# Kernel optimization log

Hardware: AMD Instinct MI355X
Metric: run time of the kernel (lower is better)

The kernel has to match this reference:

```python
import jax, jax.numpy as jnp
import numpy as np

H, DH = 16, 64            # num heads, head dim
D = H * DH                # hidden size 1024
ALPHA, BW, A, R = 1.0, 1.0, 0.5, 1.0
D_INT = DH                # num_heads > 1 -> d_intrinsic = head_dim
EPS = 1e-12
CLIP = 1.0 - 1e-6         # keep acos (and its grad) finite


def setup_inputs() -> dict:
    key = jax.random.key(0)
    ks = jax.random.split(key, 5)
    w = lambda k: jax.random.normal(k, (D, D), jnp.float32) * 0.02
    return {
        "x": jax.random.normal(ks[0], (4, 1024, D), jnp.float32),
        "wq": w(ks[1]), "bq": jnp.zeros((D,), jnp.float32),
        "wk": w(ks[2]), "bk": jnp.zeros((D,), jnp.float32),
        "wv": w(ks[3]), "bv": jnp.zeros((D,), jnp.float32),
        "wo": w(ks[4]), "bo": jnp.zeros((D,), jnp.float32),
    }


def reference(x, wq, bq, wk, bk, wv, bv, wo, bo):
    B, S, _ = x.shape

    def heads(t):  # [B,S,D] -> [B,H,S,DH]
        return t.reshape(B, S, H, DH).transpose(0, 2, 1, 3)

    def l2norm(t):
        return t / jnp.maximum(jnp.linalg.norm(t, axis=-1, keepdims=True), EPS)

    q = l2norm(heads(x @ wq + bq))
    k = l2norm(heads(x @ wk + bk))
    v = heads(x @ wv + bv)

    # spherical geodesic distance
    dot = jnp.clip(jnp.einsum('bhqd,bhkd->bhqk', q, k), -CLIP, CLIP)
    g_dist = jnp.arccos(dot) * R

    # power-law kernel (alpha < 2 branch)
    attn_score = (1.0 + g_dist / jnp.sqrt(BW)) ** (-(D_INT + ALPHA))

    # bistochastic (Sinkhorn-like) normalization, a > 0 branch
    n_r = attn_score.sum(-1)   # [B,H,S] row sums
    n_c = attn_score.sum(-2)   # [B,H,S] col sums
    k_tilde = (n_r ** (-A))[..., :, None] * attn_score * (n_c ** (-A))[..., None, :]
    probs = k_tilde / jnp.maximum(k_tilde.sum(-1, keepdims=True), EPS)  # L1 row normalize

    out = jnp.einsum('bhqk,bhkd->bhqd', probs, v)
    out = out.transpose(0, 2, 1, 3).reshape(B, S, D)
    return out @ wo + bo
```

## Files before the change

### kernel.cpp

```cpp
#include <hip/hip_runtime.h>
#include <hip/hip_bf16.h>
#include <cstdint>
#include <cstddef>

#define BATCH  4
#define SEQ    1024
#define NHEAD  16
#define DHEAD  64
#define DMODEL 1024
#define NROWS  4096
#define BH     64
#define CLIPV  0.999999f
#define PEXP   65.0f

#define QOFF   133.5f
#define QK_    490.8988764f
#define QINV   0.0020370716f
#define QC     65535.5f

typedef _Float16 h16;
typedef _Float16 half8 __attribute__((ext_vector_type(8)));
typedef _Float16 half4 __attribute__((ext_vector_type(4)));
typedef __fp16   fp16x2 __attribute__((ext_vector_type(2)));
typedef float    f32x4 __attribute__((ext_vector_type(4)));
typedef unsigned uint2v __attribute__((ext_vector_type(2)));

typedef const __attribute__((address_space(1))) void gas_void;
typedef __attribute__((address_space(3))) void las_void;
#define GLOAD_LDS16(g, l) \
    __builtin_amdgcn_global_load_lds((gas_void*)(g), (las_void*)(l), 16, 0, 0)

__device__ __forceinline__ float spfns_lg(float d) {
    d = __builtin_amdgcn_fmed3f(d, -CLIPV, CLIPV);
    float a = fabsf(d);
    float s = __builtin_amdgcn_sqrtf(1.0f - a);
    float p = -0.0187293f;
    p = fmaf(p, a,  0.0742610f);
    p = fmaf(p, a, -0.2121144f);
    p = fmaf(p, a,  1.5707288f);
    float r = s * p;
    float g = (d >= 0.0f) ? r : (3.14159265358979f - r);
    return __builtin_amdgcn_logf(1.0f + g);
}

__device__ __forceinline__ unsigned pk_h2(float lo, float hi) {
    fp16x2 v = __builtin_amdgcn_cvt_pkrtz(lo, hi);
    return __builtin_bit_cast(unsigned, v);
}

__device__ __forceinline__ half8 h8_zero() {
    half8 z;
    #pragma unroll
    for (int e = 0; e < 8; ++e) z[e] = (h16)0.f;
    return z;
}

__global__ __launch_bounds__(256) void cvt_x(const float* __restrict__ x,
                                             h16* __restrict__ xh)
{
    size_t i = ((size_t)blockIdx.x * 256 + threadIdx.x) * 8;
    float4 a = *reinterpret_cast<const float4*>(&x[i]);
    float4 b = *reinterpret_cast<const float4*>(&x[i + 4]);
    half8 o;
    o[0]=(h16)a.x; o[1]=(h16)a.y; o[2]=(h16)a.z; o[3]=(h16)a.w;
    o[4]=(h16)b.x; o[5]=(h16)b.y; o[6]=(h16)b.z; o[7]=(h16)b.w;
    *reinterpret_cast<half8*>(&xh[i]) = o;
}

__global__ __launch_bounds__(256) void wtrans(const float* __restrict__ wq,
                                              const float* __restrict__ wk,
                                              const float* __restrict__ wv,
                                              const float* __restrict__ wo,
                                              h16* __restrict__ wt3,
                                              h16* __restrict__ wot)
{
    __shared__ float T[64][65];
    const int k0 = blockIdx.x * 64, d0 = blockIdx.y * 64, z = blockIdx.z;
    const float* src = (z==0)?wq:(z==1)?wk:(z==2)?wv:wo;
    h16* dst = (z==3) ? wot : (wt3 + (size_t)z * 1024 * 1024);
    const int t = threadIdx.x;

    #pragma unroll
    for (int p = 0; p < 4; ++p) {
        int k = (t >> 4) + p * 16;
        int c = (t & 15) * 4;
        float4 v = *reinterpret_cast<const float4*>(&src[(size_t)(k0 + k) * 1024 + d0 + c]);
        T[c + 0][k] = v.x; T[c + 1][k] = v.y; T[c + 2][k] = v.z; T[c + 3][k] = v.w;
    }
    __syncthreads();
    #pragma unroll
    for (int p = 0; p < 2; ++p) {
        int dl = (t >> 3) + p * 32;
        int c  = (t & 7) * 8;
        half8 o;
        #pragma unroll
        for (int e = 0; e < 8; ++e) o[e] = (h16)T[dl][c + e];
        *reinterpret_cast<half8*>(&dst[(size_t)(d0 + dl) * 1024 + k0 + c]) = o;
    }
}

__global__ __launch_bounds__(256) void gemm_f16(const h16* __restrict__ A,
                                                const h16* __restrict__ Bt,
                                                const float* __restrict__ b0,
                                                const float* __restrict__ b1,
                                                const float* __restrict__ b2,
                                                h16* __restrict__ oq,
                                                h16* __restrict__ ok,
                                                h16* __restrict__ ovt,
                                                float* __restrict__ of32,
                                                int mode)
{
    __shared__ __align__(16) h16 As[128][64];
    __shared__ __align__(16) h16 Bs[128][64];
    const int n0 = blockIdx.x * 128, d0 = blockIdx.y * 128;
    const int t = threadIdx.x, l = t & 63, w = t >> 6;
    const int wr = (w >> 1) * 64, wc = (w & 1) * 64;
    const int lr = l >> 3, lc8 = (l & 7) * 8;

    f32x4 acc[4][4];
    #pragma unroll
    for (int i = 0; i < 4; ++i)
        #pragma unroll
        for (int j = 0; j < 4; ++j) acc[i][j] = (f32x4){0.f,0.f,0.f,0.f};

    for (int k0 = 0; k0 < 1024; k0 += 64) {
        __syncthreads();
        #pragma unroll
        for (int q = 0; q < 4; ++q) {
            int r = w * 32 + q * 8;
            GLOAD_LDS16(&A[(size_t)(n0 + r + lr) * 1024 + k0 + lc8], &As[r][0]);
            GLOAD_LDS16(&Bt[(size_t)(d0 + r + lr) * 1024 + k0 + lc8], &Bs[r][0]);
        }
        __syncthreads();
        #pragma unroll
        for (int kk = 0; kk < 2; ++kk) {
            half8 a[4], b[4];
            #pragma unroll
            for (int fi = 0; fi < 4; ++fi)
                a[fi] = *reinterpret_cast<const half8*>(&As[wr + fi*16 + (l & 15)][((l >> 4) * 8) + kk * 32]);
            #pragma unroll
            for (int fj = 0; fj < 4; ++fj)
                b[fj] = *reinterpret_cast<const half8*>(&Bs[wc + fj*16 + (l & 15)][((l >> 4) * 8) + kk * 32]);
            #pragma unroll
            for (int fi = 0; fi < 4; ++fi)
                #pragma unroll
                for (int fj = 0; fj < 4; ++fj)
                    acc[fi][fj] = __builtin_amdgcn_mfma_f32_16x16x32_f16(a[fi], b[fj], acc[fi][fj], 0, 0, 0);
        }
    }

    if (mode == 0) {
        const int dbase = d0 + wc;
        const int mat = dbase >> 10, d1b = dbase & 1023, h = d1b >> 6;
        const float* bp = (mat == 0) ? b0 : (mat == 1) ? b1 : b2;
        #pragma unroll
        for (int fi = 0; fi < 4; ++fi) {
            float vals[4][4];
            #pragma unroll
            for (int fj = 0; fj < 4; ++fj) {
                float bias = bp[d1b + fj * 16 + (l & 15)];
                #pragma unroll
                for (int rr = 0; rr < 4; ++rr) vals[fj][rr] = acc[fi][fj][rr] + bias;
            }
            if (mat < 2) {
                float ss[4];
                #pragma unroll
                for (int rr = 0; rr < 4; ++rr)
                    ss[rr] = vals[0][rr]*vals[0][rr] + vals[1][rr]*vals[1][rr]
                           + vals[2][rr]*vals[2][rr] + vals[3][rr]*vals[3][rr];
                #pragma unroll
                for (int off = 1; off < 16; off <<= 1) {
                    #pragma unroll
                    for (int rr = 0; rr < 4; ++rr) ss[rr] += __shfl_xor(ss[rr], off);
                }
                #pragma unroll
                for (int rr = 0; rr < 4; ++rr) {
                    float sc = __builtin_amdgcn_rcpf(
                        fmaxf(__builtin_amdgcn_sqrtf(ss[rr]), 1e-12f));
                    #pragma unroll
                    for (int fj = 0; fj < 4; ++fj) vals[fj][rr] *= sc;
                }
            }
            const int s0n = n0 + wr + fi * 16 + ((l >> 4) << 2);
            #pragma unroll
            for (int fj = 0; fj < 4; ++fj) {
                int dh = fj * 16 + (l & 15);
                if (mat == 2) {
                    int b = s0n >> 10, s0 = s0n & 1023;
                    half4 o;
                    #pragma unroll
                    for (int rr = 0; rr < 4; ++rr) o[rr] = (h16)vals[fj][rr];
                    *reinterpret_cast<half4*>(&ovt[(((size_t)(b * NHEAD + h)) * DHEAD + dh) * SEQ + s0]) = o;
                } else {
                    h16* dst = (mat == 0) ? oq : ok;
                    #pragma unroll
                    for (int rr = 0; rr < 4; ++rr) {
                        int n = s0n + rr, b = n >> 10, s = n & 1023;
                        dst[(((size_t)(b * NHEAD + h)) * SEQ + s) * DHEAD + dh] = (h16)vals[fj][rr];
                    }
                }
            }
        }
    } else {
        #pragma unroll
        for (int fi = 0; fi < 4; ++fi) {
            #pragma unroll
            for (int fj = 0; fj < 4; ++fj) {
                int d = d0 + wc + fj * 16 + (l & 15);
                int s0n = n0 + wr + fi * 16 + ((l >> 4) << 2);
                float bias = b0[d];
                #pragma unroll
                for (int rr = 0; rr < 4; ++rr) {
                    int n = s0n + rr;
                    of32[(size_t)n * DMODEL + d] = acc[fi][fj][rr] + bias;
                }
            }
        }
    }
}

template<int CACHED>
__global__ __launch_bounds__(256) void passA(const h16* __restrict__ qh,
                                             const h16* __restrict__ kh,
                                             float* __restrict__ nc,
                                             unsigned* __restrict__ rm_u,
                                             int* __restrict__ gacc,
                                             unsigned short* __restrict__ Sw)
{
    __shared__ __align__(16) h16 Ks[32][72];
    __shared__ float red[4][32];
    const int t = threadIdx.x, l = t & 63, w = t >> 6;
    const int id  = blockIdx.y * 32 + blockIdx.x;
    const int nid = (id & 7) * 256 + (id >> 3);
    const int jt = nid & 31, bh = nid >> 5;
    const int j0 = jt * 32;

    {
        int r = t >> 3, c = (t & 7) * 8;
        *reinterpret_cast<half8*>(&Ks[r][c]) =
            *reinterpret_cast<const half8*>(&kh[(((size_t)bh * SEQ) + j0 + r) * DHEAD + c]);
    }
    __syncthreads();

    half8 kfr[2][2];
    #pragma unroll
    for (int f = 0; f < 2; ++f)
        #pragma unroll
        for (int kk = 0; kk < 2; ++kk)
            kfr[f][kk] = *reinterpret_cast<const half8*>(&Ks[f*16 + (l & 15)][((l >> 4) * 8) + kk * 32]);

    float ncacc[8];
    #pragma unroll
    for (int x = 0; x < 8; ++x) ncacc[x] = 0.f;

    unsigned short* sp[2] = {nullptr, nullptr};
    if (CACHED) {
        size_t base = ((((size_t)(bh*16 + (jt >> 1))*16)*16 + w*4 + (jt & 1)*2) << 8)
                      + (size_t)l*4;
        sp[0] = Sw + base;
        sp[1] = sp[0] + 256;
    }

    const h16* qb = qh + ((size_t)bh * SEQ + w*16 + (l & 15)) * DHEAD + ((l >> 4) * 8);
    half8 nq0 = *reinterpret_cast<const half8*>(qb);
    half8 nq1 = *reinterpret_cast<const half8*>(qb + 32);

    #pragma unroll 2
    for (int it = 0; it < 16; ++it) {
        half8 aq0 = nq0, aq1 = nq1;
        if (it < 15) {
            const h16* qn = qb + (size_t)(it + 1) * 64 * DHEAD;
            nq0 = *reinterpret_cast<const half8*>(qn);
            nq1 = *reinterpret_cast<const half8*>(qn + 32);
        }

        float mloc = 1e30f;
        #pragma unroll
        for (int f = 0; f < 2; ++f) {
            f32x4 cfr = (f32x4){0.f,0.f,0.f,0.f};
            cfr = __builtin_amdgcn_mfma_f32_16x16x32_f16(kfr[f][0], aq0, cfr, 0, 0, 0);
            cfr = __builtin_amdgcn_mfma_f32_16x16x32_f16(kfr[f][1], aq1, cfr, 0, 0, 0);
            unsigned uq[4];
            #pragma unroll
            for (int rr = 0; rr < 4; ++rr) {
                float lg = spfns_lg(cfr[rr]);
                float tt = lg * (-PEXP);
                ncacc[f*4 + rr] += __builtin_amdgcn_exp2f(tt);
                mloc = fminf(mloc, lg);
                if (CACHED) uq[rr] = (unsigned)fmaf(tt, QK_, QC);
            }
            if (CACHED) {
                uint2v pkw;
                pkw[0] = uq[0] | (uq[1] << 16);
                pkw[1] = uq[2] | (uq[3] << 16);
                *reinterpret_cast<uint2v*>(sp[f]) = pkw;
            }
        }
        if (CACHED) { sp[0] += 4096; sp[1] += 4096; }
        mloc = fminf(mloc, __shfl_xor(mloc, 16));
        mloc = fminf(mloc, __shfl_xor(mloc, 32));
        if (l < 16)
            atomicMin(&rm_u[(size_t)bh * SEQ + it*64 + w*16 + l], __float_as_uint(mloc));
    }

    #pragma unroll
    for (int x = 0; x < 8; ++x) {
        #pragma unroll
        for (int off = 1; off < 16; off <<= 1)
            ncacc[x] += __shfl_xor(ncacc[x], off);
    }
    if ((l & 15) == 0) {
        #pragma unroll
        for (int x = 0; x < 8; ++x)
            red[w][(x >> 2) * 16 + (l >> 4) * 4 + (x & 3)] = ncacc[x];
    }
    __syncthreads();
    if (t < 32) {
        float v = red[0][t] + red[1][t] + red[2][t] + red[3][t];
        nc[(size_t)bh * SEQ + j0 + t] = v;
        atomicAdd(gacc, (int)rintf(__builtin_amdgcn_logf(v) * 64.0f));
    }
}

__global__ __launch_bounds__(256) void ncprep(const float* __restrict__ nc,
                                              const unsigned* __restrict__ rm_u,
                                              const int* __restrict__ gacc,
                                              float* __restrict__ lcr,
                                              float* __restrict__ lrm)
{
    int i = blockIdx.x * 256 + threadIdx.x;
    float Lm = (float)(*gacc) / (65536.0f * 64.0f);
    lcr[i] = -0.5f * (__builtin_amdgcn_logf(nc[i]) - Lm);
    lrm[i] = -PEXP * __uint_as_float(rm_u[i]);
}

__global__ __launch_bounds__(256) void passB_c(const h16* __restrict__ vt,
                                               const float* __restrict__ lcr,
                                               const float* __restrict__ lrm,
                                               const unsigned short* __restrict__ Sw,
                                               h16* __restrict__ aoh)
{
    __shared__ __align__(16) h16 Vs[2][64][72];
    __shared__ __align__(16) h16 Ps[4][16][72];
    const int t = threadIdx.x, l = t & 63, w = t >> 6;
    const int id  = blockIdx.y * 16 + blockIdx.x;
    const int nid = (id & 7) * 128 + (id >> 3);
    const int it = nid & 15, bh = nid >> 4;
    const int i0 = it * 64;

    const float nlr = -lrm[(size_t)bh * SEQ + i0 + w*16 + (l & 15)] - QOFF;

    half8 ones8 = h8_zero();
    if ((l & 15) == 0) {
        #pragma unroll
        for (int e = 0; e < 8; ++e) ones8[e] = (h16)1.0f;
    }

    f32x4 pv[4];
    #pragma unroll
    for (int fd = 0; fd < 4; ++fd) pv[fd] = (f32x4){0.f,0.f,0.f,0.f};
    f32x4 pvden = (f32x4){0.f,0.f,0.f,0.f};

    const int sr = t >> 3, sc = (t & 7) * 8;
    const h16* vsrc = vt + ((size_t)bh * DHEAD + sr) * SEQ + sc;
    const float* lc_base = lcr + (size_t)bh * SEQ + (l >> 4) * 4;

    auto s_ptr = [&](int jc2, int fj) -> const uint2v* {
        size_t sidx = (((((size_t)(bh*16 + jc2)*16 + it)*4 + w)*4 + fj) << 8) + (size_t)l*4;
        return reinterpret_cast<const uint2v*>(&Sw[sidx]);
    };

    half8 vr0 = *reinterpret_cast<const half8*>(vsrc);
    half8 vr1 = *reinterpret_cast<const half8*>(vsrc + (size_t)32 * SEQ);
    uint2v sv[4];
    float4 lc[4];
    #pragma unroll
    for (int fj = 0; fj < 4; ++fj) {
        sv[fj] = *s_ptr(0, fj);
        lc[fj] = *reinterpret_cast<const float4*>(&lc_base[fj*16]);
    }

    int pb = 0;
    for (int jc = 0; jc < 16; ++jc) {
        *reinterpret_cast<half8*>(&Vs[pb][sr][sc])      = vr0;
        *reinterpret_cast<half8*>(&Vs[pb][sr + 32][sc]) = vr1;

        if (jc < 15) {
            const h16* vn = vsrc + (jc + 1) * 64;
            vr0 = *reinterpret_cast<const half8*>(vn);
            vr1 = *reinterpret_cast<const half8*>(vn + (size_t)32 * SEQ);
        }
        __syncthreads();

        #pragma unroll
        for (int fj = 0; fj < 4; ++fj) {
            float u0 = (float)(sv[fj][0] & 0xffffu), u1 = (float)(sv[fj][0] >> 16);
            float u2 = (float)(sv[fj][1] & 0xffffu), u3 = (float)(sv[fj][1] >> 16);
            float pp0 = __builtin_amdgcn_exp2f(fmaf(u0, QINV, lc[fj].x + nlr));
            float pp1 = __builtin_amdgcn_exp2f(fmaf(u1, QINV, lc[fj].y + nlr));
            float pp2 = __builtin_amdgcn_exp2f(fmaf(u2, QINV, lc[fj].z + nlr));
            float pp3 = __builtin_amdgcn_exp2f(fmaf(u3, QINV, lc[fj].w + nlr));
            uint2v pk;
            pk[0] = pk_h2(pp0, pp1);
            pk[1] = pk_h2(pp2, pp3);
            *reinterpret_cast<uint2v*>(&Ps[w][l & 15][fj*16 + (l >> 4) * 4]) = pk;
        }
        if (jc < 15) {
            #pragma unroll
            for (int fj = 0; fj < 4; ++fj) {
                sv[fj] = *s_ptr(jc + 1, fj);
                lc[fj] = *reinterpret_cast<const float4*>(&lc_base[(jc + 1)*64 + fj*16]);
            }
        }

        half8 pa0 = *reinterpret_cast<const half8*>(&Ps[w][l & 15][((l >> 4) * 8)]);
        half8 pa1 = *reinterpret_cast<const half8*>(&Ps[w][l & 15][((l >> 4) * 8) + 32]);
        #pragma unroll
        for (int fd = 0; fd < 4; ++fd) {
            half8 vb0 = *reinterpret_cast<const half8*>(&Vs[pb][fd*16 + (l & 15)][((l >> 4) * 8)]);
            half8 vb1 = *reinterpret_cast<const half8*>(&Vs[pb][fd*16 + (l & 15)][((l >> 4) * 8) + 32]);
            pv[fd] = __builtin_amdgcn_mfma_f32_16x16x32_f16(pa0, vb0, pv[fd], 0, 0, 0);
            pv[fd] = __builtin_amdgcn_mfma_f32_16x16x32_f16(pa1, vb1, pv[fd], 0, 0, 0);
        }
        pvden = __builtin_amdgcn_mfma_f32_16x16x32_f16(pa0, ones8, pvden, 0, 0, 0);
        pvden = __builtin_amdgcn_mfma_f32_16x16x32_f16(pa1, ones8, pvden, 0, 0, 0);
        pb ^= 1;
    }

    const int b = bh >> 4, h = bh & 15;
    #pragma unroll
    for (int rr = 0; rr < 4; ++rr) {
        float ds = __shfl(pvden[rr], l & 48);
        float inv = __builtin_amdgcn_rcpf(ds);
        int s = i0 + w * 16 + ((l >> 4) << 2) + rr;
        #pragma unroll
        for (int fd = 0; fd < 4; ++fd) {
            aoh[((size_t)(b * SEQ + s)) * DMODEL + h * DHEAD + fd * 16 + (l & 15)] =
                (h16)(pv[fd][rr] * inv);
        }
    }
}

__global__ __launch_bounds__(256) void passB_r(const h16* __restrict__ qh,
                                               const h16* __restrict__ kh,
                                               const h16* __restrict__ vt,
                                               const float* __restrict__ lcr,
                                               const float* __restrict__ lrm,
                                               h16* __restrict__ aoh)
{
    __shared__ __align__(16) h16 Ks[64][72];
    __shared__ __align__(16) h16 Vs[64][72];
    __shared__ __align__(16) h16 Ps[4][16][72];
    __shared__ float lcr_s[64];
    __shared__ float lrm_s[64];

    const int it = blockIdx.x, bh = blockIdx.y;
    const int i0 = it * 64;
    const int t = threadIdx.x, l = t & 63, w = t >> 6;
    h16* Pflat = &Ps[0][0][0];

    #pragma unroll
    for (int p = 0; p < 2; ++p) {
        int r = (t >> 3) + p * 32, c = (t & 7) * 8;
        *reinterpret_cast<half8*>(&Pflat[r * 72 + c]) =
            *reinterpret_cast<const half8*>(&qh[(((size_t)bh * SEQ) + i0 + r) * DHEAD + c]);
    }
    if (t < 64) lrm_s[t] = lrm[(size_t)bh * SEQ + i0 + t];
    __syncthreads();

    half8 aq0 = *reinterpret_cast<const half8*>(&Pflat[(w*16 + (l & 15)) * 72 + ((l >> 4) * 8)]);
    half8 aq1 = *reinterpret_cast<const half8*>(&Pflat[(w*16 + (l & 15)) * 72 + ((l >> 4) * 8) + 32]);
    const float nlr = -lrm_s[w*16 + (l & 15)];

    half8 ones8 = h8_zero();
    if ((l & 15) == 0) {
        #pragma unroll
        for (int e = 0; e < 8; ++e) ones8[e] = (h16)1.0f;
    }

    f32x4 pv[4];
    #pragma unroll
    for (int fd = 0; fd < 4; ++fd) pv[fd] = (f32x4){0.f,0.f,0.f,0.f};
    f32x4 pvden = (f32x4){0.f,0.f,0.f,0.f};

    for (int jc = 0; jc < 16; ++jc) {
        const int j0 = jc * 64;
        __syncthreads();
        #pragma unroll
        for (int p = 0; p < 2; ++p) {
            int r = (t >> 3) + p * 32, c = (t & 7) * 8;
            *reinterpret_cast<half8*>(&Ks[r][c]) =
                *reinterpret_cast<const half8*>(&kh[(((size_t)bh * SEQ) + j0 + r) * DHEAD + c]);
            *reinterpret_cast<half8*>(&Vs[r][c]) =
                *reinterpret_cast<const half8*>(&vt[(((size_t)bh * DHEAD) + r) * SEQ + j0 + c]);
        }
        if (t < 64) lcr_s[t] = lcr[(size_t)bh * SEQ + j0 + t];
        __syncthreads();

        #pragma unroll
        for (int fj = 0; fj < 4; ++fj) {
            half8 kb0 = *reinterpret_cast<const half8*>(&Ks[fj*16 + (l & 15)][((l >> 4) * 8)]);
            half8 kb1 = *reinterpret_cast<const half8*>(&Ks[fj*16 + (l & 15)][((l >> 4) * 8) + 32]);
            f32x4 cfr = (f32x4){0.f,0.f,0.f,0.f};
            cfr = __builtin_amdgcn_mfma_f32_16x16x32_f16(kb0, aq0, cfr, 0, 0, 0);
            cfr = __builtin_amdgcn_mfma_f32_16x16x32_f16(kb1, aq1, cfr, 0, 0, 0);
            float4 lc4 = *reinterpret_cast<const float4*>(&lcr_s[fj*16 + (l >> 4) * 4]);
            float pp0 = __builtin_amdgcn_exp2f(fmaf(spfns_lg(cfr[0]), -PEXP, lc4.x + nlr));
            float pp1 = __builtin_amdgcn_exp2f(fmaf(spfns_lg(cfr[1]), -PEXP, lc4.y + nlr));
            float pp2 = __builtin_amdgcn_exp2f(fmaf(spfns_lg(cfr[2]), -PEXP, lc4.z + nlr));
            float pp3 = __builtin_amdgcn_exp2f(fmaf(spfns_lg(cfr[3]), -PEXP, lc4.w + nlr));
            uint2v pk;
            pk[0] = pk_h2(pp0, pp1);
            pk[1] = pk_h2(pp2, pp3);
            *reinterpret_cast<uint2v*>(&Ps[w][l & 15][fj*16 + (l >> 4) * 4]) = pk;
        }

        half8 pa0 = *reinterpret_cast<const half8*>(&Ps[w][l & 15][((l >> 4) * 8)]);
        half8 pa1 = *reinterpret_cast<const half8*>(&Ps[w][l & 15][((l >> 4) * 8) + 32]);
        #pragma unroll
        for (int fd = 0; fd < 4; ++fd) {
            half8 vb0 = *reinterpret_cast<const half8*>(&Vs[fd*16 + (l & 15)][((l >> 4) * 8)]);
            half8 vb1 = *reinterpret_cast<const half8*>(&Vs[fd*16 + (l & 15)][((l >> 4) * 8) + 32]);
            pv[fd] = __builtin_amdgcn_mfma_f32_16x16x32_f16(pa0, vb0, pv[fd], 0, 0, 0);
            pv[fd] = __builtin_amdgcn_mfma_f32_16x16x32_f16(pa1, vb1, pv[fd], 0, 0, 0);
        }
        pvden = __builtin_amdgcn_mfma_f32_16x16x32_f16(pa0, ones8, pvden, 0, 0, 0);
        pvden = __builtin_amdgcn_mfma_f32_16x16x32_f16(pa1, ones8, pvden, 0, 0, 0);
    }

    const int b = bh >> 4, h = bh & 15;
    #pragma unroll
    for (int rr = 0; rr < 4; ++rr) {
        float ds = __shfl(pvden[rr], l & 48);
        float inv = __builtin_amdgcn_rcpf(ds);
        int s = i0 + w * 16 + ((l >> 4) << 2) + rr;
        #pragma unroll
        for (int fd = 0; fd < 4; ++fd) {
            aoh[((size_t)(b * SEQ + s)) * DMODEL + h * DHEAD + fd * 16 + (l & 15)] =
                (h16)(pv[fd][rr] * inv);
        }
    }
}

extern "C" void kernel_launch(void* const* d_in, const int* in_sizes, int n_in,
                              void* d_out, int out_size, void* d_ws, size_t ws_size,
                              hipStream_t stream)
{
    (void)in_sizes; (void)n_in; (void)out_size;
    const float* x  = (const float*)d_in[0];
    const float* wq = (const float*)d_in[1];
    const float* bq = (const float*)d_in[2];
    const float* wk = (const float*)d_in[3];
    const float* bk = (const float*)d_in[4];
    const float* wv = (const float*)d_in[5];
    const float* bv = (const float*)d_in[6];
    const float* wo = (const float*)d_in[7];
    const float* bo = (const float*)d_in[8];
    float* out = (float*)d_out;

    h16* ws16 = (h16*)d_ws;
    const size_t NX  = (size_t)NROWS * DMODEL;
    const size_t NW3 = (size_t)3 * DMODEL * DMODEL;
    const size_t NW1 = (size_t)DMODEL * DMODEL;
    const size_t NH  = (size_t)BH * SEQ * DHEAD;
    h16* xh  = ws16;
    h16* wt3 = xh  + NX;
    h16* wot = wt3 + NW3;
    h16* qh  = wot + NW1;
    h16* kh  = qh  + NH;
    h16* vt  = kh  + NH;
    h16* aoh = vt  + NH;
    float* nc  = (float*)(aoh + NX);
    float* lcr = nc  + BH * SEQ;
    float* lrm = lcr + BH * SEQ;
    unsigned* rm_u = (unsigned*)(lrm + BH * SEQ);
    int* gacc = (int*)(rm_u + BH * SEQ);

    size_t used = (size_t)((char*)(gacc + 1) - (char*)d_ws);
    used = (used + 255) & ~(size_t)255;
    unsigned short* Sw = (unsigned short*)((char*)d_ws + used);
    const size_t SBYTES = (size_t)BH * SEQ * SEQ * 2;
    const bool cache = (ws_size >= used + SBYTES);

    hipMemsetAsync(rm_u, 0xFF, (size_t)BH * SEQ * sizeof(unsigned), stream);
    hipMemsetAsync(gacc, 0, sizeof(int), stream);

    cvt_x<<<2048, 256, 0, stream>>>(x, xh);
    wtrans<<<dim3(16, 16, 4), 256, 0, stream>>>(wq, wk, wv, wo, wt3, wot);

    gemm_f16<<<dim3(32, 24), 256, 0, stream>>>(xh, wt3, bq, bk, bv,
                                               qh, kh, vt, nullptr, 0);

    if (cache) {
        passA<1><<<dim3(32, BH), 256, 0, stream>>>(qh, kh, nc, rm_u, gacc, Sw);
        ncprep<<<256, 256, 0, stream>>>(nc, rm_u, gacc, lcr, lrm);
        passB_c<<<dim3(16, BH), 256, 0, stream>>>(vt, lcr, lrm, Sw, aoh);
    } else {
        passA<0><<<dim3(32, BH), 256, 0, stream>>>(qh, kh, nc, rm_u, gacc, Sw);
        ncprep<<<256, 256, 0, stream>>>(nc, rm_u, gacc, lcr, lrm);
        passB_r<<<dim3(16, BH), 256, 0, stream>>>(qh, kh, vt, lcr, lrm, aoh);
    }

    gemm_f16<<<dim3(32, 8), 256, 0, stream>>>(aoh, wot, bo, nullptr, nullptr,
                                              nullptr, nullptr, nullptr, out, 1);
}
```

Baseline: 181.3 us.

## Split cached PV pass over key halves and merge partial results

The cached attention-value pass is split into two halves along the key dimension, doubling the grid to 2048 blocks. Each half writes unnormalized fp16 partial outputs and fp32 row denominators to scratch, reusing the q buffer as storage. A new merge kernel sums the two halves, normalizes, and writes the head-interleaved output. This trades an extra launch and partial-sum traffic, plus fp16 rounding of the partials and a single-buffered V tile with an extra barrier, for more parallelism and occupancy.

Measured after the change: 185.9 us. 1.03x slower.

```diff
diff --git a/kernel.cpp b/kernel.cpp
--- a/kernel.cpp
+++ b/kernel.cpp
@@ -334,19 +334,21 @@
     lrm[i] = -PEXP * __uint_as_float(rm_u[i]);
 }
 
-__global__ __launch_bounds__(256) void passB_c(const h16* __restrict__ vt,
-                                               const float* __restrict__ lcr,
-                                               const float* __restrict__ lrm,
-                                               const unsigned short* __restrict__ Sw,
-                                               h16* __restrict__ aoh)
-{
-    __shared__ __align__(16) h16 Vs[2][64][72];
+__global__ __launch_bounds__(256) void passB_c2(const h16* __restrict__ vt,
+                                                const float* __restrict__ lcr,
+                                                const float* __restrict__ lrm,
+                                                const unsigned short* __restrict__ Sw,
+                                                h16* __restrict__ pvp,
+                                                float* __restrict__ denp)
+{
+    __shared__ __align__(16) h16 Vs[64][72];
     __shared__ __align__(16) h16 Ps[4][16][72];
     const int t = threadIdx.x, l = t & 63, w = t >> 6;
-    const int id  = blockIdx.y * 16 + blockIdx.x;
-    const int nid = (id & 7) * 128 + (id >> 3);
-    const int it = nid & 15, bh = nid >> 4;
+    const int id  = blockIdx.y * 32 + blockIdx.x;
+    const int nid = (id & 7) * 256 + (id >> 3);
+    const int jh = nid & 1, it = (nid >> 1) & 15, bh = nid >> 5;
     const int i0 = it * 64;
+    const int jc0 = jh * 8;
 
     const float nlr = -lrm[(size_t)bh * SEQ + i0 + w*16 + (l & 15)] - QOFF;
 
@@ -370,27 +372,27 @@
         return reinterpret_cast<const uint2v*>(&Sw[sidx]);
     };
 
-    half8 vr0 = *reinterpret_cast<const half8*>(vsrc);
-    half8 vr1 = *reinterpret_cast<const half8*>(vsrc + (size_t)32 * SEQ);
+    half8 vr0 = *reinterpret_cast<const half8*>(vsrc + jc0 * 64);
+    half8 vr1 = *reinterpret_cast<const half8*>(vsrc + jc0 * 64 + (size_t)32 * SEQ);
     uint2v sv[4];
     float4 lc[4];
     #pragma unroll
     for (int fj = 0; fj < 4; ++fj) {
-        sv[fj] = *s_ptr(0, fj);
-        lc[fj] = *reinterpret_cast<const float4*>(&lc_base[fj*16]);
-    }
-
-    int pb = 0;
-    for (int jc = 0; jc < 16; ++jc) {
-        *reinterpret_cast<half8*>(&Vs[pb][sr][sc])      = vr0;
-        *reinterpret_cast<half8*>(&Vs[pb][sr + 32][sc]) = vr1;
-
-        if (jc < 15) {
+        sv[fj] = *s_ptr(jc0, fj);
+        lc[fj] = *reinterpret_cast<const float4*>(&lc_base[jc0*64 + fj*16]);
+    }
+
+    for (int jc = jc0; jc < jc0 + 8; ++jc) {
+        __syncthreads();
+        *reinterpret_cast<half8*>(&Vs[sr][sc])      = vr0;
+        *reinterpret_cast<half8*>(&Vs[sr + 32][sc]) = vr1;
+        __syncthreads();
+
+        if (jc < jc0 + 7) {
             const h16* vn = vsrc + (jc + 1) * 64;
             vr0 = *reinterpret_cast<const half8*>(vn);
             vr1 = *reinterpret_cast<const half8*>(vn + (size_t)32 * SEQ);
         }
-        __syncthreads();
 
         #pragma unroll
         for (int fj = 0; fj < 4; ++fj) {
@@ -405,7 +407,7 @@
             pk[1] = pk_h2(pp2, pp3);
             *reinterpret_cast<uint2v*>(&Ps[w][l & 15][fj*16 + (l >> 4) * 4]) = pk;
         }
-        if (jc < 15) {
+        if (jc < jc0 + 7) {
             #pragma unroll
             for (int fj = 0; fj < 4; ++fj) {
                 sv[fj] = *s_ptr(jc + 1, fj);
@@ -417,28 +419,53 @@
         half8 pa1 = *reinterpret_cast<const half8*>(&Ps[w][l & 15][((l >> 4) * 8) + 32]);
         #pragma unroll
         for (int fd = 0; fd < 4; ++fd) {
-            half8 vb0 = *reinterpret_cast<const half8*>(&Vs[pb][fd*16 + (l & 15)][((l >> 4) * 8)]);
-            half8 vb1 = *reinterpret_cast<const half8*>(&Vs[pb][fd*16 + (l & 15)][((l >> 4) * 8) + 32]);
+            half8 vb0 = *reinterpret_cast<const half8*>(&Vs[fd*16 + (l & 15)][((l >> 4) * 8)]);
+            half8 vb1 = *reinterpret_cast<const half8*>(&Vs[fd*16 + (l & 15)][((l >> 4) * 8) + 32]);
             pv[fd] = __builtin_amdgcn_mfma_f32_16x16x32_f16(pa0, vb0, pv[fd], 0, 0, 0);
             pv[fd] = __builtin_amdgcn_mfma_f32_16x16x32_f16(pa1, vb1, pv[fd], 0, 0, 0);
         }
         pvden = __builtin_amdgcn_mfma_f32_16x16x32_f16(pa0, ones8, pvden, 0, 0, 0);
         pvden = __builtin_amdgcn_mfma_f32_16x16x32_f16(pa1, ones8, pvden, 0, 0, 0);
-        pb ^= 1;
-    }
-
+    }
+
+    const int blk = (bh * 16 + it) * 2 + jh;
+    #pragma unroll
+    for (int rr = 0; rr < 4; ++rr) {
+        int row = w * 16 + ((l >> 4) << 2) + rr;
+        #pragma unroll
+        for (int fd = 0; fd < 4; ++fd)
+            pvp[(size_t)blk * 4096 + row * 64 + fd * 16 + (l & 15)] = (h16)pv[fd][rr];
+        if ((l & 15) == 0)
+            denp[blk * 64 + row] = pvden[rr];
+    }
+}
+
+__global__ __launch_bounds__(256) void mergePV(const h16* __restrict__ pvp,
+                                               const float* __restrict__ denp,
+                                               h16* __restrict__ aoh)
+{
+    const int bi = blockIdx.x;
+    const int bh = bi >> 4, it = bi & 15;
+    const int t = threadIdx.x;
+    const int rl = t >> 2, dq = (t & 3) * 16;
+    const size_t base0 = (size_t)(bi * 2 + 0) * 4096 + (size_t)rl * 64 + dq;
+    const size_t base1 = (size_t)(bi * 2 + 1) * 4096 + (size_t)rl * 64 + dq;
+    half8 a0 = *reinterpret_cast<const half8*>(&pvp[base0]);
+    half8 a1 = *reinterpret_cast<const half8*>(&pvp[base0 + 8]);
+    half8 b0 = *reinterpret_cast<const half8*>(&pvp[base1]);
+    half8 b1 = *reinterpret_cast<const half8*>(&pvp[base1 + 8]);
+    float den = denp[(bi * 2) * 64 + rl] + denp[(bi * 2 + 1) * 64 + rl];
+    float inv = __builtin_amdgcn_rcpf(den);
+    half8 o0, o1;
+    #pragma unroll
+    for (int e = 0; e < 8; ++e) {
+        o0[e] = (h16)(((float)a0[e] + (float)b0[e]) * inv);
+        o1[e] = (h16)(((float)a1[e] + (float)b1[e]) * inv);
+    }
     const int b = bh >> 4, h = bh & 15;
-    #pragma unroll
-    for (int rr = 0; rr < 4; ++rr) {
-        float ds = __shfl(pvden[rr], l & 48);
-        float inv = __builtin_amdgcn_rcpf(ds);
-        int s = i0 + w * 16 + ((l >> 4) << 2) + rr;
-        #pragma unroll
-        for (int fd = 0; fd < 4; ++fd) {
-            aoh[((size_t)(b * SEQ + s)) * DMODEL + h * DHEAD + fd * 16 + (l & 15)] =
-                (h16)(pv[fd][rr] * inv);
-        }
-    }
+    size_t dst = ((size_t)(b * SEQ + it * 64 + rl)) * DMODEL + h * DHEAD + dq;
+    *reinterpret_cast<half8*>(&aoh[dst])     = o0;
+    *reinterpret_cast<half8*>(&aoh[dst + 8]) = o1;
 }
 
 __global__ __launch_bounds__(256) void passB_r(const h16* __restrict__ qh,
@@ -575,13 +602,16 @@
     float* lrm = lcr + BH * SEQ;
     unsigned* rm_u = (unsigned*)(lrm + BH * SEQ);
     int* gacc = (int*)(rm_u + BH * SEQ);
-
-    size_t used = (size_t)((char*)(gacc + 1) - (char*)d_ws);
+    float* denp = (float*)(gacc + 1);
+
+    size_t used = (size_t)((char*)(denp + 2 * 1024 * 64) - (char*)d_ws);
     used = (used + 255) & ~(size_t)255;
     unsigned short* Sw = (unsigned short*)((char*)d_ws + used);
     const size_t SBYTES = (size_t)BH * SEQ * SEQ * 2;
     const bool cache = (ws_size >= used + SBYTES);
 
+    h16* pvp = qh;
+
     hipMemsetAsync(rm_u, 0xFF, (size_t)BH * SEQ * sizeof(unsigned), stream);
     hipMemsetAsync(gacc, 0, sizeof(int), stream);
 
@@ -594,7 +624,8 @@
     if (cache) {
         passA<1><<<dim3(32, BH), 256, 0, stream>>>(qh, kh, nc, rm_u, gacc, Sw);
         ncprep<<<256, 256, 0, stream>>>(nc, rm_u, gacc, lcr, lrm);
-        passB_c<<<dim3(16, BH), 256, 0, stream>>>(vt, lcr, lrm, Sw, aoh);
+        passB_c2<<<dim3(32, BH), 256, 0, stream>>>(vt, lcr, lrm, Sw, pvp, denp);
+        mergePV<<<1024, 256, 0, stream>>>(pvp, denp, aoh);
     } else {
         passA<0><<<dim3(32, BH), 256, 0, stream>>>(qh, kh, nc, rm_u, gacc, Sw);
         ncprep<<<256, 256, 0, stream>>>(nc, rm_u, gacc, lcr, lrm);
```
